# Optimization experiments

Hardware: AMD Instinct MI355X
Metric: run time of the kernel (lower is better)

## Reference

```python
import jax, jax.numpy as jnp
import numpy as np


def _linear_init(key, fan_in, fan_out):
    bound = 1.0 / np.sqrt(fan_in)
    k1, k2 = jax.random.split(key)
    w = jax.random.uniform(k1, (fan_in, fan_out), jnp.float32, -bound, bound)
    b = jax.random.uniform(k2, (fan_out,), jnp.float32, -bound, bound)
    return w, b


def setup_inputs() -> dict:
    key = jax.random.key(0)
    ks = jax.random.split(key, 8)
    B, T, K, F, H, D = 4, 64, 50, 6, 128, 256
    states = jax.random.normal(ks[0], (B, T, K, F), jnp.float32)
    masks = (jax.random.uniform(ks[1], (B, T, K)) < 0.9).astype(jnp.float32)
    w_a, b_a = _linear_init(ks[2], F, H)              # agent_encoder
    w_r1, b_r1 = _linear_init(ks[3], 2 * H + 3, H)    # relation_encoder layer 1
    w_r2, b_r2 = _linear_init(ks[4], H, H)            # relation_encoder layer 2
    w_g, b_g = _linear_init(ks[5], 2 * H, H)          # graph_aggregation
    w_f1, b_f1 = _linear_init(ks[6], H, D)            # final_encoder layer 1
    w_f2, b_f2 = _linear_init(ks[7], D, D)            # final_encoder layer 2
    return dict(states=states, masks=masks, w_a=w_a, b_a=b_a,
                w_r1=w_r1, b_r1=b_r1, w_r2=w_r2, b_r2=b_r2,
                w_g=w_g, b_g=b_g, w_f1=w_f1, b_f1=b_f1, w_f2=w_f2, b_f2=b_f2)


def _safe_norm(r):
    # sqrt(sum r^2) with well-defined gradient at 0 (torch.norm convention)
    sq = jnp.sum(r * r, axis=-1, keepdims=True)
    return jnp.where(sq == 0, 0.0, jnp.sqrt(jnp.where(sq == 0, 1.0, sq)))


def reference(states, masks, w_a, b_a, w_r1, b_r1, w_r2, b_r2,
              w_g, b_g, w_f1, b_f1, w_f2, b_f2):
    B, T, K, F = states.shape
    H = w_a.shape[1]
    s = states.reshape(B * T, K, F)            # [N,K,F]
    m = masks.reshape(B * T, K)                # [N,K]
    agent_feat = jax.nn.relu(s @ w_a + b_a)    # [N,K,H] (dropout = identity, eval)
    pos = s[..., :2]
    vel = s[..., 2:4]
    # rel[n,i,j] = quantity_j - quantity_i
    rel_pos = pos[:, None, :, :] - pos[:, :, None, :]   # [N,K,K,2]
    rel_vel = vel[:, None, :, :] - vel[:, :, None, :]
    dist = _safe_norm(rel_pos)                          # [N,K,K,1]
    rx, ry = rel_pos[..., 0:1], rel_pos[..., 1:2]
    safe_x = jnp.where((rx == 0) & (ry == 0), 1.0, rx)  # atan2(0,1)=atan2(0,0)=0
    angle = jnp.arctan2(ry, safe_x)
    speed_diff = _safe_norm(rel_vel)
    geo = jnp.concatenate([dist, angle, speed_diff], axis=-1)  # [N,K,K,3]
    # Split the first relation linear instead of materializing the
    # [N,K,K,2H+3] concat: cat([f_i, f_j, geo]) @ w_r1 == f@w_i + f@w_j + geo@w_geo
    x_i = agent_feat @ w_r1[:H]            # [N,K,H]
    x_j = agent_feat @ w_r1[H:2 * H]       # [N,K,H]
    g = geo @ w_r1[2 * H:] + b_r1          # [N,K,K,H]
    h = jax.nn.relu(x_i[:, :, None, :] + x_j[:, None, :, :] + g)
    rel_feat = h @ w_r2 + b_r2             # [N,K,K,H]
    mask_pairs = m[:, :, None] * m[:, None, :]          # [N,i,j]
    rel_feat = rel_feat * mask_pairs[..., None]
    denom = jnp.maximum(mask_pairs.sum(axis=2, keepdims=True), 1.0)  # [N,K,1]
    agg = rel_feat.sum(axis=2) / denom                  # [N,K,H]
    combined = jax.nn.relu(agent_feat @ w_g[:H] + agg @ w_g[H:] + b_g)  # [N,K,H]
    me = m[..., None]
    pooled = (combined * me).sum(axis=1) / jnp.maximum(me.sum(axis=1), 1.0)  # [N,H]
    latent = jax.nn.relu(pooled @ w_f1 + b_f1) @ w_f2 + b_f2                 # [N,D]
    return latent.reshape(B, T, -1)
```

## Files before the change

### kernel.cpp

```cpp
#include <hip/hip_runtime.h>

#define KA 50
#define KP 52
#define H 128
#define D 256
#define NBLK 256
#define BLOCK 1024
#define NG 8
#define RPT 7
#define STRD 136

#define WS_WI 0
#define WS_WJ 32
#define WS_WR2 64
#define WS_WG 96
#define NFRAG 160

typedef __attribute__((ext_vector_type(8))) short bf16x8;
typedef __attribute__((ext_vector_type(4))) float f32x4;
typedef __attribute__((ext_vector_type(2))) float v2f;

__device__ __forceinline__ float bf2f(unsigned short u) {
  return __uint_as_float(((unsigned)u) << 16);
}
__device__ __forceinline__ unsigned short f2bf(float f) {
  unsigned u = __float_as_uint(f);
  u = (u + 0x7FFFu + ((u >> 16) & 1u)) >> 16;
  return (unsigned short)u;
}
__device__ __forceinline__ int rli(int v, int l) {
  return __builtin_amdgcn_readlane(v, l);
}

__global__ void pack_weights(const float* __restrict__ w_r1,
                             const float* __restrict__ w_r2,
                             const float* __restrict__ w_g,
                             unsigned short* __restrict__ wp) {
  const int t = blockIdx.x * 256 + threadIdx.x;
  if (t >= NFRAG * 64) return;
  const int f = t >> 6, lane = t & 63;
  const float* W; int rowbase, sf;
  if (f < 64)       { W = w_r1; rowbase = (f < 32) ? 0 : 128; sf = f & 31; }
  else if (f < 96)  { W = w_r2; rowbase = 0; sf = f - 64; }
  else              { W = w_g;  rowbase = 0; sf = f - 96; }
  const int kt = sf >> 3, ctl = sf & 7;
  const int col = ctl * 16 + (lane & 15);
  const int k0  = rowbase + kt * 32 + (lane >> 4) * 8;
  unsigned short v[8];
  #pragma unroll
  for (int j = 0; j < 8; ++j) v[j] = f2bf(W[(k0 + j) * H + col]);
  #pragma unroll
  for (int j = 0; j < 8; ++j) wp[(size_t)t * 8 + j] = v[j];
}

struct alignas(16) Smem {
  unsigned short af[KP * STRD];
  unsigned short xi[KP * STRD];
  unsigned short xj[KP * H];
  unsigned short hsum[KP * STRD];
  float red[1024];
  float pooled[H];
  float latent1[D];
  float s[KA][6];
  float m[64];
  float cnta[KP];
  float invden[KP];
  float cnt;
};

__global__ void __launch_bounds__(BLOCK) rpe_kernel(
    const float* __restrict__ states, const float* __restrict__ masks,
    const float* __restrict__ w_a,  const float* __restrict__ b_a,
    const float* __restrict__ w_r1, const float* __restrict__ b_r1,
    const float* __restrict__ b_r2,
    const float* __restrict__ b_g,
    const float* __restrict__ w_f1, const float* __restrict__ b_f1,
    const float* __restrict__ w_f2, const float* __restrict__ b_f2,
    const unsigned short* __restrict__ wp,
    float* __restrict__ out) {
  __shared__ Smem sh;
  const int n = blockIdx.x;
  const int tid = threadIdx.x;
  const int c = tid & (H - 1);
  const int bg = tid >> 7;
  const int wid = tid >> 6, lane = tid & 63;
  const int ct = wid & 7;
  const int rtb = (wid >> 3) * 2;
  const int fr = lane & 15;
  const int fkg = lane >> 4;
  const int col = ct * 16 + fr;

  const float bac = b_a[c];
  const float wa0 = w_a[0*H+c], wa1 = w_a[1*H+c], wa2 = w_a[2*H+c];
  const float wa3 = w_a[3*H+c], wa4 = w_a[4*H+c], wa5 = w_a[5*H+c];
  const int c0 = 2 * lane;
  const v2f wgd01  = { w_r1[256*H + c0], w_r1[256*H + c0+1] };
  const v2f wgan01 = { w_r1[257*H + c0], w_r1[257*H + c0+1] };
  const v2f wgs01  = { w_r1[258*H + c0], w_r1[258*H + c0+1] };
  const v2f br101  = { b_r1[c0], b_r1[c0+1] };

  {
    if (tid < KA * 6) ((float*)sh.s)[tid] = states[(size_t)n * (KA * 6) + tid];
    if (tid < 64) sh.m[tid] = (tid < KA) ? masks[(size_t)n * KA + tid] : 0.f;
    if (tid < 2 * H) {
      const int r5 = KA + (tid >> 7), cc = tid & (H - 1);
      sh.af[r5 * STRD + cc] = 0;
      sh.hsum[r5 * STRD + cc] = 0;
    }
  }
  __syncthreads();
  if (wid == 0) {
    float v = sh.m[lane];
    v += __shfl_xor(v, 1);  v += __shfl_xor(v, 2);  v += __shfl_xor(v, 4);
    v += __shfl_xor(v, 8);  v += __shfl_xor(v, 16); v += __shfl_xor(v, 32);
    if (lane == 0) sh.cnt = v;
  }

  const int bl = (lane < KA) ? lane : (KA - 1);
  const float pbx = sh.s[bl][0], pby = sh.s[bl][1];
  const float pvx = sh.s[bl][2], pvy = sh.s[bl][3];
  const unsigned mbits = (sh.m[lane] != 0.f) ? 0x3F800000u : 0u;
  unsigned q0[3], q1[3];
  #pragma unroll
  for (int r = 0; r < 3; ++r) {
    const int ar = wid + 16 * r;
    const float rx  = pbx - sh.s[ar][0], ry  = pby - sh.s[ar][1];
    const float dvx = pvx - sh.s[ar][2], dvy = pvy - sh.s[ar][3];
    const float dist = sqrtf(fmaf(rx, rx, ry * ry));
    const float sx = (rx == 0.f && ry == 0.f) ? 1.f : rx;
    const float ang = atan2f(ry, sx);
    const float sd  = sqrtf(fmaf(dvx, dvx, dvy * dvy));
    q0[r] = (unsigned)f2bf(dist) | ((unsigned)f2bf(ang) << 16);
    q1[r] = (unsigned)f2bf(sd) | mbits;
  }
  unsigned q0t = 0, q1t = 0;
  if (wid < 2) {
    const int ar = 48 + wid;
    const float rx  = pbx - sh.s[ar][0], ry  = pby - sh.s[ar][1];
    const float dvx = pvx - sh.s[ar][2], dvy = pvy - sh.s[ar][3];
    const float dist = sqrtf(fmaf(rx, rx, ry * ry));
    const float sx = (rx == 0.f && ry == 0.f) ? 1.f : rx;
    const float ang = atan2f(ry, sx);
    const float sd  = sqrtf(fmaf(dvx, dvx, dvy * dvy));
    q0t = (unsigned)f2bf(dist) | ((unsigned)f2bf(ang) << 16);
    q1t = (unsigned)f2bf(sd) | mbits;
  }

  {
    #pragma unroll
    for (int r = 0; r < RPT; ++r) {
      const int a = bg + NG * r;
      if (a < KA) {
        const float* srow = sh.s[a];
        float v = fmaf(srow[0], wa0, fmaf(srow[1], wa1, fmaf(srow[2], wa2,
                  fmaf(srow[3], wa3, fmaf(srow[4], wa4, fmaf(srow[5], wa5, bac))))));
        sh.af[a * STRD + c] = f2bf(fmaxf(v, 0.f));
      }
    }
  }
  bf16x8 Bi[4], Bj[4];
  #pragma unroll
  for (int kt = 0; kt < 4; ++kt) {
    Bi[kt] = *(const bf16x8*)&wp[(size_t)((WS_WI + kt*8 + ct) * 64 + lane) * 8];
    Bj[kt] = *(const bf16x8*)&wp[(size_t)((WS_WJ + kt*8 + ct) * 64 + lane) * 8];
  }
  __syncthreads();
  if (tid < KP) {
    const float ca = (tid < KA) ? sh.m[tid] * sh.cnt : 0.f;
    sh.cnta[tid] = ca;
    sh.invden[tid] = 1.0f / fmaxf(ca, 1.0f);
  }

  {
    f32x4 ci0 = {0,0,0,0}, ci1 = {0,0,0,0}, cj0 = {0,0,0,0}, cj1 = {0,0,0,0};
    #pragma unroll
    for (int kt = 0; kt < 4; ++kt) {
      const bf16x8 A0 = *(const bf16x8*)&sh.af[(rtb*16 + fr) * STRD + kt*32 + fkg*8];
      const bf16x8 A1 = *(const bf16x8*)&sh.af[((rtb+1)*16 + fr) * STRD + kt*32 + fkg*8];
      ci0 = __builtin_amdgcn_mfma_f32_16x16x32_bf16(A0, Bi[kt], ci0, 0, 0, 0);
      ci1 = __builtin_amdgcn_mfma_f32_16x16x32_bf16(A1, Bi[kt], ci1, 0, 0, 0);
      cj0 = __builtin_amdgcn_mfma_f32_16x16x32_bf16(A0, Bj[kt], cj0, 0, 0, 0);
      cj1 = __builtin_amdgcn_mfma_f32_16x16x32_bf16(A1, Bj[kt], cj1, 0, 0, 0);
    }
    #pragma unroll
    for (int rt2 = 0; rt2 < 2; ++rt2) {
      const f32x4 vi = rt2 ? ci1 : ci0;
      const f32x4 vj = rt2 ? cj1 : cj0;
      #pragma unroll
      for (int g = 0; g < 4; ++g) {
        const int r = (rtb + rt2) * 16 + fkg * 4 + g;
        if (r < KP) {
          sh.xi[r * STRD + col] = f2bf(vi[g]);
          sh.xj[r * H + col]    = f2bf(vj[g]);
        }
      }
    }
  }
  __syncthreads();

  {
    v2f base01[3], acc01[3];
    #pragma unroll
    for (int r = 0; r < 3; ++r) {
      const int ar = wid + 16 * r;
      const unsigned xip = *(const unsigned*)&sh.xi[ar * STRD + c0];
      base01[r] = (v2f){ bf2f((unsigned short)xip), bf2f((unsigned short)(xip >> 16)) } + br101;
      acc01[r] = (v2f){0.f, 0.f};
    }
    #pragma unroll 10
    for (int b = 0; b < KA; ++b) {
      const unsigned xjp = *(const unsigned*)&sh.xj[b * H + c0];
      const v2f xj01 = { __uint_as_float(xjp << 16),
                         __uint_as_float(xjp & 0xFFFF0000u) };
      #pragma unroll
      for (int r = 0; r < 3; ++r) {
        const unsigned rq0 = (unsigned)rli((int)q0[r], b);
        const unsigned rq1 = (unsigned)rli((int)q1[r], b);
        const float dd = __uint_as_float(rq0 << 16);
        const float aa = __uint_as_float(rq0 & 0xFFFF0000u);
        const float ss = __uint_as_float(rq1 << 16);
        const float mm = __uint_as_float(rq1 & 0xFFFF0000u);
        v2f t = __builtin_elementwise_fma((v2f){dd, dd}, wgd01, base01[r] + xj01);
        t = __builtin_elementwise_fma((v2f){aa, aa}, wgan01, t);
        t = __builtin_elementwise_fma((v2f){ss, ss}, wgs01, t);
        t = __builtin_elementwise_max(t, (v2f){0.f, 0.f});
        acc01[r] = __builtin_elementwise_fma((v2f){mm, mm}, t, acc01[r]);
      }
    }
    #pragma unroll
    for (int r = 0; r < 3; ++r) {
      const int ar = wid + 16 * r;
      const float ma = sh.m[ar];
      *(unsigned*)&sh.hsum[ar * STRD + c0] =
          (unsigned)f2bf(acc01[r].x * ma) | ((unsigned)f2bf(acc01[r].y * ma) << 16);
    }
    if (wid < 2) {
      const int ar = 48 + wid;
      const unsigned xip = *(const unsigned*)&sh.xi[ar * STRD + c0];
      const v2f baset = (v2f){ bf2f((unsigned short)xip),
                               bf2f((unsigned short)(xip >> 16)) } + br101;
      v2f acct = {0.f, 0.f};
      #pragma unroll 10
      for (int b = 0; b < KA; ++b) {
        const unsigned xjp = *(const unsigned*)&sh.xj[b * H + c0];
        const v2f xj01 = { __uint_as_float(xjp << 16),
                           __uint_as_float(xjp & 0xFFFF0000u) };
        const unsigned rq0 = (unsigned)rli((int)q0t, b);
        const unsigned rq1 = (unsigned)rli((int)q1t, b);
        const float dd = __uint_as_float(rq0 << 16);
        const float aa = __uint_as_float(rq0 & 0xFFFF0000u);
        const float ss = __uint_as_float(rq1 << 16);
        const float mm = __uint_as_float(rq1 & 0xFFFF0000u);
        v2f t = __builtin_elementwise_fma((v2f){dd, dd}, wgd01, baset + xj01);
        t = __builtin_elementwise_fma((v2f){aa, aa}, wgan01, t);
        t = __builtin_elementwise_fma((v2f){ss, ss}, wgs01, t);
        t = __builtin_elementwise_max(t, (v2f){0.f, 0.f});
        acct = __builtin_elementwise_fma((v2f){mm, mm}, t, acct);
      }
      const float ma = sh.m[ar];
      *(unsigned*)&sh.hsum[ar * STRD + c0] =
          (unsigned)f2bf(acct.x * ma) | ((unsigned)f2bf(acct.y * ma) << 16);
    }
  }
  __syncthreads();

  f32x4 p0 = {0,0,0,0}, p1 = {0,0,0,0};
  {
    f32x4 a0 = {0,0,0,0}, a1 = {0,0,0,0};
    #pragma unroll
    for (int kt = 0; kt < 4; ++kt) {
      const bf16x8 B4 = *(const bf16x8*)&wp[(size_t)((WS_WR2 + kt*8 + ct) * 64 + lane) * 8];
      const bf16x8 A0h = *(const bf16x8*)&sh.hsum[(rtb*16 + fr) * STRD + kt*32 + fkg*8];
      const bf16x8 A1h = *(const bf16x8*)&sh.hsum[((rtb+1)*16 + fr) * STRD + kt*32 + fkg*8];
      a0 = __builtin_amdgcn_mfma_f32_16x16x32_bf16(A0h, B4, a0, 0, 0, 0);
      a1 = __builtin_amdgcn_mfma_f32_16x16x32_bf16(A1h, B4, a1, 0, 0, 0);
      const bf16x8 B5 = *(const bf16x8*)&wp[(size_t)((WS_WG + kt*8 + ct) * 64 + lane) * 8];
      const bf16x8 A0a = *(const bf16x8*)&sh.af[(rtb*16 + fr) * STRD + kt*32 + fkg*8];
      const bf16x8 A1a = *(const bf16x8*)&sh.af[((rtb+1)*16 + fr) * STRD + kt*32 + fkg*8];
      p0 = __builtin_amdgcn_mfma_f32_16x16x32_bf16(A0a, B5, p0, 0, 0, 0);
      p1 = __builtin_amdgcn_mfma_f32_16x16x32_bf16(A1a, B5, p1, 0, 0, 0);
    }
    const float br2c = b_r2[col];
    #pragma unroll
    for (int rt2 = 0; rt2 < 2; ++rt2) {
      const f32x4 v = rt2 ? a1 : a0;
      #pragma unroll
      for (int g = 0; g < 4; ++g) {
        const int r = (rtb + rt2) * 16 + fkg * 4 + g;
        if (r < KP) {
          const float val = fmaf(sh.cnta[r], br2c, v[g]) * sh.invden[r];
          sh.xi[r * STRD + col] = f2bf(val);
        }
      }
    }
  }
  __syncthreads();

  {
    #pragma unroll
    for (int kt = 0; kt < 4; ++kt) {
      const bf16x8 B = *(const bf16x8*)&wp[(size_t)((WS_WG + (kt+4)*8 + ct) * 64 + lane) * 8];
      const bf16x8 A0 = *(const bf16x8*)&sh.xi[(rtb*16 + fr) * STRD + kt*32 + fkg*8];
      const bf16x8 A1 = *(const bf16x8*)&sh.xi[((rtb+1)*16 + fr) * STRD + kt*32 + fkg*8];
      p0 = __builtin_amdgcn_mfma_f32_16x16x32_bf16(A0, B, p0, 0, 0, 0);
      p1 = __builtin_amdgcn_mfma_f32_16x16x32_bf16(A1, B, p1, 0, 0, 0);
    }
    const float bgc = b_g[col];
    float pv = 0.f;
    #pragma unroll
    for (int rt2 = 0; rt2 < 2; ++rt2) {
      const f32x4 v = rt2 ? p1 : p0;
      #pragma unroll
      for (int g = 0; g < 4; ++g) {
        const int r = (rtb + rt2) * 16 + fkg * 4 + g;
        if (r < KA) {
          pv = fmaf(sh.m[r], fmaxf(v[g] + bgc, 0.f), pv);
        }
      }
    }
    pv += __shfl_xor(pv, 16);
    pv += __shfl_xor(pv, 32);
    if (lane < 16) sh.red[(wid >> 3) * H + col] = pv;
  }
  __syncthreads();
  if (tid < H) {
    const float invp = 1.0f / fmaxf(sh.cnt, 1.0f);
    sh.pooled[tid] = (sh.red[tid] + sh.red[H + tid]) * invp;
  }
  __syncthreads();

  {
    const int d  = tid & (D - 1);
    const int hh = tid >> 8;
    const float* wf = w_f1 + d;
    float acc = 0.f;
    const int k0 = hh * 32;
    #pragma unroll 8
    for (int k = 0; k < 32; ++k)
      acc = fmaf(sh.pooled[k0 + k], wf[(k0 + k) * D], acc);
    sh.red[hh * D + d] = acc;
  }
  __syncthreads();
  if (tid < D) {
    sh.latent1[tid] = fmaxf(sh.red[tid] + sh.red[D + tid] +
                            sh.red[2*D + tid] + sh.red[3*D + tid] +
                            b_f1[tid], 0.f);
  }
  __syncthreads();

  {
    const int d  = tid & (D - 1);
    const int hh = tid >> 8;
    const float* wf = w_f2 + d;
    float acc = 0.f;
    const int k0 = hh * 64;
    #pragma unroll 8
    for (int k = 0; k < 64; ++k)
      acc = fmaf(sh.latent1[k0 + k], wf[(k0 + k) * D], acc);
    sh.red[hh * D + d] = acc;
  }
  __syncthreads();
  if (tid < D) {
    out[(size_t)n * D + tid] = sh.red[tid] + sh.red[D + tid] +
                               sh.red[2*D + tid] + sh.red[3*D + tid] +
                               b_f2[tid];
  }
}

extern "C" void kernel_launch(void* const* d_in, const int* in_sizes, int n_in,
                              void* d_out, int out_size, void* d_ws, size_t ws_size,
                              hipStream_t stream) {
  const float* states = (const float*)d_in[0];
  const float* masks  = (const float*)d_in[1];
  const float* w_a  = (const float*)d_in[2];
  const float* b_a  = (const float*)d_in[3];
  const float* w_r1 = (const float*)d_in[4];
  const float* b_r1 = (const float*)d_in[5];
  const float* w_r2 = (const float*)d_in[6];
  const float* b_r2 = (const float*)d_in[7];
  const float* w_g  = (const float*)d_in[8];
  const float* b_g  = (const float*)d_in[9];
  const float* w_f1 = (const float*)d_in[10];
  const float* b_f1 = (const float*)d_in[11];
  const float* w_f2 = (const float*)d_in[12];
  const float* b_f2 = (const float*)d_in[13];
  float* out = (float*)d_out;
  unsigned short* wp = (unsigned short*)d_ws;

  hipLaunchKernelGGL(pack_weights, dim3((NFRAG * 64 + 255) / 256), dim3(256), 0, stream,
                     w_r1, w_r2, w_g, wp);
  hipLaunchKernelGGL(rpe_kernel, dim3(NBLK), dim3(BLOCK), 0, stream,
                     states, masks, w_a, b_a, w_r1, b_r1, b_r2,
                     b_g, w_f1, b_f1, w_f2, b_f2, wp, out);
}
```

Measured before the change: 37.73 us.

## Split per-sample work across two 512-thread blocks and move final MLP to separate kernel

The single 1024-thread block per sample becomes two 512-thread blocks. Each block handles half of the agent rows for the pairwise relation stage and recomputes the full x_j projection redundantly. Partial pooled sums and the mask count go to a workspace, and a second kernel runs the final two-layer MLP. The aim is more blocks for better CU occupancy on 256 CUs, at the cost of redundant agent-encoder and x_j work, an extra kernel launch, and a global-memory round trip.

```diff
diff --git a/kernel.cpp b/kernel.cpp
--- a/kernel.cpp
+++ b/kernel.cpp
@@ -4,10 +4,6 @@
 #define KP 52
 #define H 128
 #define D 256
-#define NBLK 256
-#define BLOCK 1024
-#define NG 8
-#define RPT 7
 #define STRD 136
 
 #define WS_WI 0
@@ -15,6 +11,8 @@
 #define WS_WR2 64
 #define WS_WG 96
 #define NFRAG 160
+#define WP_BYTES (NFRAG * 512 * 2)
+#define PP_STRIDE 260
 
 typedef __attribute__((ext_vector_type(8))) short bf16x8;
 typedef __attribute__((ext_vector_type(4))) float f32x4;
@@ -53,14 +51,12 @@
   for (int j = 0; j < 8; ++j) wp[(size_t)t * 8 + j] = v[j];
 }
 
-struct alignas(16) Smem {
+struct alignas(16) SmemA {
   unsigned short af[KP * STRD];
   unsigned short xi[KP * STRD];
   unsigned short xj[KP * H];
   unsigned short hsum[KP * STRD];
-  float red[1024];
-  float pooled[H];
-  float latent1[D];
+  float red[H];
   float s[KA][6];
   float m[64];
   float cnta[KP];
@@ -68,27 +64,27 @@
   float cnt;
 };
 
-__global__ void __launch_bounds__(BLOCK) rpe_kernel(
+__global__ void __launch_bounds__(512) rpe_a(
     const float* __restrict__ states, const float* __restrict__ masks,
     const float* __restrict__ w_a,  const float* __restrict__ b_a,
     const float* __restrict__ w_r1, const float* __restrict__ b_r1,
-    const float* __restrict__ b_r2,
-    const float* __restrict__ b_g,
-    const float* __restrict__ w_f1, const float* __restrict__ b_f1,
-    const float* __restrict__ w_f2, const float* __restrict__ b_f2,
+    const float* __restrict__ b_r2, const float* __restrict__ b_g,
     const unsigned short* __restrict__ wp,
-    float* __restrict__ out) {
-  __shared__ Smem sh;
-  const int n = blockIdx.x;
+    float* __restrict__ pp) {
+  __shared__ SmemA sh;
+  const int bid = blockIdx.x;
+  const int n = bid >> 1, h = bid & 1;
   const int tid = threadIdx.x;
   const int c = tid & (H - 1);
-  const int bg = tid >> 7;
+  const int rg = tid >> 7;
   const int wid = tid >> 6, lane = tid & 63;
-  const int ct = wid & 7;
-  const int rtb = (wid >> 3) * 2;
+  const int ct = wid;
+  const int rtb = h * 2;
   const int fr = lane & 15;
   const int fkg = lane >> 4;
   const int col = ct * 16 + fr;
+  const int rowbase = h * 32;
+  const int NR = 4 - 2 * h;
 
   const float bac = b_a[c];
   const float wa0 = w_a[0*H+c], wa1 = w_a[1*H+c], wa2 = w_a[2*H+c];
@@ -120,10 +116,10 @@
   const float pbx = sh.s[bl][0], pby = sh.s[bl][1];
   const float pvx = sh.s[bl][2], pvy = sh.s[bl][3];
   const unsigned mbits = (sh.m[lane] != 0.f) ? 0x3F800000u : 0u;
-  unsigned q0[3], q1[3];
+  unsigned q0[4] = {0,0,0,0}, q1[4] = {0,0,0,0};
   #pragma unroll
-  for (int r = 0; r < 3; ++r) {
-    const int ar = wid + 16 * r;
+  for (int r = 0; r < 4; ++r) if (r < NR) {
+    const int ar = rowbase + r * 8 + wid;
     const float rx  = pbx - sh.s[ar][0], ry  = pby - sh.s[ar][1];
     const float dvx = pvx - sh.s[ar][2], dvy = pvy - sh.s[ar][3];
     const float dist = sqrtf(fmaf(rx, rx, ry * ry));
@@ -134,7 +130,7 @@
     q1[r] = (unsigned)f2bf(sd) | mbits;
   }
   unsigned q0t = 0, q1t = 0;
-  if (wid < 2) {
+  if (h == 1 && wid < 2) {
     const int ar = 48 + wid;
     const float rx  = pbx - sh.s[ar][0], ry  = pby - sh.s[ar][1];
     const float dvx = pvx - sh.s[ar][2], dvy = pvy - sh.s[ar][3];
@@ -148,8 +144,8 @@
 
   {
     #pragma unroll
-    for (int r = 0; r < RPT; ++r) {
-      const int a = bg + NG * r;
+    for (int r = 0; r < 13; ++r) {
+      const int a = rg + 4 * r;
       if (a < KA) {
         const float* srow = sh.s[a];
         float v = fmaf(srow[0], wa0, fmaf(srow[1], wa1, fmaf(srow[2], wa2,
@@ -172,40 +168,53 @@
   }
 
   {
-    f32x4 ci0 = {0,0,0,0}, ci1 = {0,0,0,0}, cj0 = {0,0,0,0}, cj1 = {0,0,0,0};
+    f32x4 cj[4] = {{0,0,0,0},{0,0,0,0},{0,0,0,0},{0,0,0,0}};
+    f32x4 ci0 = {0,0,0,0}, ci1 = {0,0,0,0};
     #pragma unroll
     for (int kt = 0; kt < 4; ++kt) {
-      const bf16x8 A0 = *(const bf16x8*)&sh.af[(rtb*16 + fr) * STRD + kt*32 + fkg*8];
-      const bf16x8 A1 = *(const bf16x8*)&sh.af[((rtb+1)*16 + fr) * STRD + kt*32 + fkg*8];
-      ci0 = __builtin_amdgcn_mfma_f32_16x16x32_bf16(A0, Bi[kt], ci0, 0, 0, 0);
-      ci1 = __builtin_amdgcn_mfma_f32_16x16x32_bf16(A1, Bi[kt], ci1, 0, 0, 0);
-      cj0 = __builtin_amdgcn_mfma_f32_16x16x32_bf16(A0, Bj[kt], cj0, 0, 0, 0);
-      cj1 = __builtin_amdgcn_mfma_f32_16x16x32_bf16(A1, Bj[kt], cj1, 0, 0, 0);
-    }
-    #pragma unroll
-    for (int rt2 = 0; rt2 < 2; ++rt2) {
-      const f32x4 vi = rt2 ? ci1 : ci0;
-      const f32x4 vj = rt2 ? cj1 : cj0;
+      bf16x8 A[4];
+      #pragma unroll
+      for (int rt = 0; rt < 4; ++rt)
+        A[rt] = *(const bf16x8*)&sh.af[(rt*16 + fr) * STRD + kt*32 + fkg*8];
+      #pragma unroll
+      for (int rt = 0; rt < 4; ++rt)
+        cj[rt] = __builtin_amdgcn_mfma_f32_16x16x32_bf16(A[rt], Bj[kt], cj[rt], 0, 0, 0);
+      const bf16x8 Ai0 = h ? A[2] : A[0];
+      const bf16x8 Ai1 = h ? A[3] : A[1];
+      ci0 = __builtin_amdgcn_mfma_f32_16x16x32_bf16(Ai0, Bi[kt], ci0, 0, 0, 0);
+      ci1 = __builtin_amdgcn_mfma_f32_16x16x32_bf16(Ai1, Bi[kt], ci1, 0, 0, 0);
+    }
+    #pragma unroll
+    for (int rt = 0; rt < 4; ++rt) {
       #pragma unroll
       for (int g = 0; g < 4; ++g) {
-        const int r = (rtb + rt2) * 16 + fkg * 4 + g;
-        if (r < KP) {
-          sh.xi[r * STRD + col] = f2bf(vi[g]);
-          sh.xj[r * H + col]    = f2bf(vj[g]);
-        }
-      }
-    }
-  }
-  __syncthreads();
-
-  {
-    v2f base01[3], acc01[3];
-    #pragma unroll
-    for (int r = 0; r < 3; ++r) {
-      const int ar = wid + 16 * r;
-      const unsigned xip = *(const unsigned*)&sh.xi[ar * STRD + c0];
-      base01[r] = (v2f){ bf2f((unsigned short)xip), bf2f((unsigned short)(xip >> 16)) } + br101;
-      acc01[r] = (v2f){0.f, 0.f};
+        const int r = rt * 16 + fkg * 4 + g;
+        if (r < KP) sh.xj[r * H + col] = f2bf(cj[rt][g]);
+      }
+    }
+    #pragma unroll
+    for (int t = 0; t < 2; ++t) {
+      const f32x4 v = t ? ci1 : ci0;
+      #pragma unroll
+      for (int g = 0; g < 4; ++g) {
+        const int r = (rtb + t) * 16 + fkg * 4 + g;
+        if (r < KP) sh.xi[r * STRD + col] = f2bf(v[g]);
+      }
+    }
+  }
+  __syncthreads();
+
+  {
+    v2f base01[4], acc01[4];
+    #pragma unroll
+    for (int r = 0; r < 4; ++r) {
+      base01[r] = (v2f){0.f, 0.f}; acc01[r] = (v2f){0.f, 0.f};
+      if (r < NR) {
+        const int ar = rowbase + r * 8 + wid;
+        const unsigned xip = *(const unsigned*)&sh.xi[ar * STRD + c0];
+        base01[r] = (v2f){ bf2f((unsigned short)xip),
+                           bf2f((unsigned short)(xip >> 16)) } + br101;
+      }
     }
     #pragma unroll 10
     for (int b = 0; b < KA; ++b) {
@@ -213,7 +222,7 @@
       const v2f xj01 = { __uint_as_float(xjp << 16),
                          __uint_as_float(xjp & 0xFFFF0000u) };
       #pragma unroll
-      for (int r = 0; r < 3; ++r) {
+      for (int r = 0; r < 4; ++r) if (r < NR) {
         const unsigned rq0 = (unsigned)rli((int)q0[r], b);
         const unsigned rq1 = (unsigned)rli((int)q1[r], b);
         const float dd = __uint_as_float(rq0 << 16);
@@ -228,13 +237,13 @@
       }
     }
     #pragma unroll
-    for (int r = 0; r < 3; ++r) {
-      const int ar = wid + 16 * r;
+    for (int r = 0; r < 4; ++r) if (r < NR) {
+      const int ar = rowbase + r * 8 + wid;
       const float ma = sh.m[ar];
       *(unsigned*)&sh.hsum[ar * STRD + c0] =
           (unsigned)f2bf(acc01[r].x * ma) | ((unsigned)f2bf(acc01[r].y * ma) << 16);
     }
-    if (wid < 2) {
+    if (h == 1 && wid < 2) {
       const int ar = 48 + wid;
       const unsigned xip = *(const unsigned*)&sh.xi[ar * STRD + c0];
       const v2f baset = (v2f){ bf2f((unsigned short)xip),
@@ -264,29 +273,29 @@
   }
   __syncthreads();
 
-  f32x4 p0 = {0,0,0,0}, p1 = {0,0,0,0};
-  {
-    f32x4 a0 = {0,0,0,0}, a1 = {0,0,0,0};
+  f32x4 p50 = {0,0,0,0}, p51 = {0,0,0,0};
+  {
+    f32x4 a40 = {0,0,0,0}, a41 = {0,0,0,0};
     #pragma unroll
     for (int kt = 0; kt < 4; ++kt) {
       const bf16x8 B4 = *(const bf16x8*)&wp[(size_t)((WS_WR2 + kt*8 + ct) * 64 + lane) * 8];
       const bf16x8 A0h = *(const bf16x8*)&sh.hsum[(rtb*16 + fr) * STRD + kt*32 + fkg*8];
       const bf16x8 A1h = *(const bf16x8*)&sh.hsum[((rtb+1)*16 + fr) * STRD + kt*32 + fkg*8];
-      a0 = __builtin_amdgcn_mfma_f32_16x16x32_bf16(A0h, B4, a0, 0, 0, 0);
-      a1 = __builtin_amdgcn_mfma_f32_16x16x32_bf16(A1h, B4, a1, 0, 0, 0);
+      a40 = __builtin_amdgcn_mfma_f32_16x16x32_bf16(A0h, B4, a40, 0, 0, 0);
+      a41 = __builtin_amdgcn_mfma_f32_16x16x32_bf16(A1h, B4, a41, 0, 0, 0);
       const bf16x8 B5 = *(const bf16x8*)&wp[(size_t)((WS_WG + kt*8 + ct) * 64 + lane) * 8];
       const bf16x8 A0a = *(const bf16x8*)&sh.af[(rtb*16 + fr) * STRD + kt*32 + fkg*8];
       const bf16x8 A1a = *(const bf16x8*)&sh.af[((rtb+1)*16 + fr) * STRD + kt*32 + fkg*8];
-      p0 = __builtin_amdgcn_mfma_f32_16x16x32_bf16(A0a, B5, p0, 0, 0, 0);
-      p1 = __builtin_amdgcn_mfma_f32_16x16x32_bf16(A1a, B5, p1, 0, 0, 0);
+      p50 = __builtin_amdgcn_mfma_f32_16x16x32_bf16(A0a, B5, p50, 0, 0, 0);
+      p51 = __builtin_amdgcn_mfma_f32_16x16x32_bf16(A1a, B5, p51, 0, 0, 0);
     }
     const float br2c = b_r2[col];
     #pragma unroll
-    for (int rt2 = 0; rt2 < 2; ++rt2) {
-      const f32x4 v = rt2 ? a1 : a0;
+    for (int t = 0; t < 2; ++t) {
+      const f32x4 v = t ? a41 : a40;
       #pragma unroll
       for (int g = 0; g < 4; ++g) {
-        const int r = (rtb + rt2) * 16 + fkg * 4 + g;
+        const int r = (rtb + t) * 16 + fkg * 4 + g;
         if (r < KP) {
           const float val = fmaf(sh.cnta[r], br2c, v[g]) * sh.invden[r];
           sh.xi[r * STRD + col] = f2bf(val);
@@ -302,69 +311,72 @@
       const bf16x8 B = *(const bf16x8*)&wp[(size_t)((WS_WG + (kt+4)*8 + ct) * 64 + lane) * 8];
       const bf16x8 A0 = *(const bf16x8*)&sh.xi[(rtb*16 + fr) * STRD + kt*32 + fkg*8];
       const bf16x8 A1 = *(const bf16x8*)&sh.xi[((rtb+1)*16 + fr) * STRD + kt*32 + fkg*8];
-      p0 = __builtin_amdgcn_mfma_f32_16x16x32_bf16(A0, B, p0, 0, 0, 0);
-      p1 = __builtin_amdgcn_mfma_f32_16x16x32_bf16(A1, B, p1, 0, 0, 0);
+      p50 = __builtin_amdgcn_mfma_f32_16x16x32_bf16(A0, B, p50, 0, 0, 0);
+      p51 = __builtin_amdgcn_mfma_f32_16x16x32_bf16(A1, B, p51, 0, 0, 0);
     }
     const float bgc = b_g[col];
     float pv = 0.f;
     #pragma unroll
-    for (int rt2 = 0; rt2 < 2; ++rt2) {
-      const f32x4 v = rt2 ? p1 : p0;
+    for (int t = 0; t < 2; ++t) {
+      const f32x4 v = t ? p51 : p50;
       #pragma unroll
       for (int g = 0; g < 4; ++g) {
-        const int r = (rtb + rt2) * 16 + fkg * 4 + g;
-        if (r < KA) {
-          pv = fmaf(sh.m[r], fmaxf(v[g] + bgc, 0.f), pv);
-        }
+        const int r = (rtb + t) * 16 + fkg * 4 + g;
+        if (r < KA) pv = fmaf(sh.m[r], fmaxf(v[g] + bgc, 0.f), pv);
       }
     }
     pv += __shfl_xor(pv, 16);
     pv += __shfl_xor(pv, 32);
-    if (lane < 16) sh.red[(wid >> 3) * H + col] = pv;
-  }
-  __syncthreads();
+    if (lane < 16) sh.red[col] = pv;
+  }
+  __syncthreads();
+  if (tid < H) pp[(size_t)n * PP_STRIDE + h * H + tid] = sh.red[tid];
+  if (h == 0 && tid == 0) pp[(size_t)n * PP_STRIDE + 256] = sh.cnt;
+}
+
+__global__ void __launch_bounds__(512) rpe_b(
+    const float* __restrict__ w_f1, const float* __restrict__ b_f1,
+    const float* __restrict__ w_f2, const float* __restrict__ b_f2,
+    const float* __restrict__ pp, float* __restrict__ out) {
+  __shared__ float pooled[H];
+  __shared__ float latent[D];
+  __shared__ float red[2 * D];
+  const int n = blockIdx.x;
+  const int tid = threadIdx.x;
+  const int d = tid & (D - 1);
+  const int hh = tid >> 8;
+
   if (tid < H) {
-    const float invp = 1.0f / fmaxf(sh.cnt, 1.0f);
-    sh.pooled[tid] = (sh.red[tid] + sh.red[H + tid]) * invp;
-  }
-  __syncthreads();
-
-  {
-    const int d  = tid & (D - 1);
-    const int hh = tid >> 8;
+    const float cnt = pp[(size_t)n * PP_STRIDE + 256];
+    const float invp = 1.0f / fmaxf(cnt, 1.0f);
+    pooled[tid] = (pp[(size_t)n * PP_STRIDE + tid] +
+                   pp[(size_t)n * PP_STRIDE + H + tid]) * invp;
+  }
+  __syncthreads();
+  {
     const float* wf = w_f1 + d;
-    float acc = 0.f;
-    const int k0 = hh * 32;
-    #pragma unroll 8
-    for (int k = 0; k < 32; ++k)
-      acc = fmaf(sh.pooled[k0 + k], wf[(k0 + k) * D], acc);
-    sh.red[hh * D + d] = acc;
-  }
-  __syncthreads();
-  if (tid < D) {
-    sh.latent1[tid] = fmaxf(sh.red[tid] + sh.red[D + tid] +
-                            sh.red[2*D + tid] + sh.red[3*D + tid] +
-                            b_f1[tid], 0.f);
-  }
-  __syncthreads();
-
-  {
-    const int d  = tid & (D - 1);
-    const int hh = tid >> 8;
-    const float* wf = w_f2 + d;
     float acc = 0.f;
     const int k0 = hh * 64;
     #pragma unroll 8
     for (int k = 0; k < 64; ++k)
-      acc = fmaf(sh.latent1[k0 + k], wf[(k0 + k) * D], acc);
-    sh.red[hh * D + d] = acc;
-  }
-  __syncthreads();
-  if (tid < D) {
-    out[(size_t)n * D + tid] = sh.red[tid] + sh.red[D + tid] +
-                               sh.red[2*D + tid] + sh.red[3*D + tid] +
-                               b_f2[tid];
-  }
+      acc = fmaf(pooled[k0 + k], wf[(k0 + k) * D], acc);
+    red[hh * D + d] = acc;
+  }
+  __syncthreads();
+  if (tid < D) latent[tid] = fmaxf(red[tid] + red[D + tid] + b_f1[tid], 0.f);
+  __syncthreads();
+  {
+    const float* wf = w_f2 + d;
+    float acc = 0.f;
+    const int k0 = hh * 128;
+    #pragma unroll 8
+    for (int k = 0; k < 128; ++k)
+      acc = fmaf(latent[k0 + k], wf[(k0 + k) * D], acc);
+    red[hh * D + d] = acc;
+  }
+  __syncthreads();
+  if (tid < D)
+    out[(size_t)n * D + tid] = red[tid] + red[D + tid] + b_f2[tid];
 }
 
 extern "C" void kernel_launch(void* const* d_in, const int* in_sizes, int n_in,
@@ -386,10 +398,12 @@
   const float* b_f2 = (const float*)d_in[13];
   float* out = (float*)d_out;
   unsigned short* wp = (unsigned short*)d_ws;
+  float* ppws = (float*)((char*)d_ws + WP_BYTES);
 
   hipLaunchKernelGGL(pack_weights, dim3((NFRAG * 64 + 255) / 256), dim3(256), 0, stream,
                      w_r1, w_r2, w_g, wp);
-  hipLaunchKernelGGL(rpe_kernel, dim3(NBLK), dim3(BLOCK), 0, stream,
-                     states, masks, w_a, b_a, w_r1, b_r1, b_r2,
-                     b_g, w_f1, b_f1, w_f2, b_f2, wp, out);
-}
+  hipLaunchKernelGGL(rpe_a, dim3(512), dim3(512), 0, stream,
+                     states, masks, w_a, b_a, w_r1, b_r1, b_r2, b_g, wp, ppws);
+  hipLaunchKernelGGL(rpe_b, dim3(256), dim3(512), 0, stream,
+                     w_f1, b_f1, w_f2, b_f2, ppws, out);
+}
```

Result: slower. 43.55 us (+15.4%).
